# Kernel optimization log

Measured on AMD Instinct MI355X. Metric: run time of the kernel, lower is better.

## Reference

```python
import jax, jax.numpy as jnp
import numpy as np

B, S, IN, H, E, OUT = 64, 2048, 256, 512, 256, 32000


def setup_inputs() -> dict:
    key = jax.random.key(0)
    ks = jax.random.split(key, 20)
    g = lambda k, shp, fan_in: jax.random.normal(k, shp, jnp.float32) / jnp.sqrt(jnp.float32(fan_in))
    return {
        "x": jax.random.normal(ks[0], (B, IN), jnp.float32),
        "hidden": jax.random.normal(ks[1], (B, H), jnp.float32),
        "encoder_outputs": jax.random.normal(ks[2], (B, S, H), jnp.float32),
        # attention params
        "W1_w": g(ks[3], (H, E), H), "W1_b": jnp.zeros((E,), jnp.float32),
        "W2_w": g(ks[4], (H, E), H),
        "v_w": g(ks[5], (E, 1), E),
        # GRU gate params (input to gates is concat(x, context): IN+H)
        "Wxr_w": g(ks[6], (IN + H, H), IN + H), "Wxr_b": jnp.zeros((H,), jnp.float32),
        "Whr_w": g(ks[7], (H, H), H),
        "Wxz_w": g(ks[8], (IN + H, H), IN + H), "Wxz_b": jnp.zeros((H,), jnp.float32),
        "Whz_w": g(ks[9], (H, H), H),
        "Wxh_w": g(ks[10], (IN + H, H), IN + H), "Wxh_b": jnp.zeros((H,), jnp.float32),
        "Whh_w": g(ks[11], (H, H), H),
        # output projection
        "Who_w": g(ks[12], (H, OUT), H), "Who_b": jnp.zeros((OUT,), jnp.float32),
    }


def reference(x, hidden, encoder_outputs,
              W1_w, W1_b, W2_w, v_w,
              Wxr_w, Wxr_b, Whr_w,
              Wxz_w, Wxz_b, Whz_w,
              Wxh_w, Wxh_b, Whh_w,
              Who_w, Who_b):
    # Bahdanau attention
    # energy: [B, S, E]
    energy = jnp.tanh(jnp.einsum("bsh,he->bse", encoder_outputs, W1_w) + W1_b
                      + (hidden @ W2_w)[:, None, :])
    scores = jnp.einsum("bse,eo->bs", energy, v_w)          # [B, S]
    attn_weights = jax.nn.softmax(scores, axis=1)            # [B, S]
    context = jnp.einsum("bs,bsh->bh", attn_weights, encoder_outputs)  # [B, H]

    x_context = jnp.concatenate([x, context], axis=-1)       # [B, IN+H]
    reset_gate = jax.nn.sigmoid(x_context @ Wxr_w + Wxr_b + hidden @ Whr_w)
    update_gate = jax.nn.sigmoid(x_context @ Wxz_w + Wxz_b + hidden @ Whz_w)
    h_tilde = jnp.tanh(x_context @ Wxh_w + Wxh_b + (reset_gate * hidden) @ Whh_w)
    new_hidden = update_gate * hidden + (1.0 - update_gate) * h_tilde
    output = new_hidden @ Who_w + Who_b                      # [B, OUT]
    return (output, new_hidden, attn_weights)
```

## Files before the change

### kernel.cpp

```cpp
#include <hip/hip_runtime.h>

#define BB 64
#define SS 2048
#define INDIM 256
#define HH 512
#define EE 256
#define OUTD 32000

typedef __attribute__((ext_vector_type(8))) short short8;
typedef __attribute__((ext_vector_type(4))) float floatx4;

#define LOG2E 1.4426950408889634f

__device__ __forceinline__ unsigned short f2bf(float f) {
  unsigned u = __float_as_uint(f);
  return (unsigned short)((u + 0x7FFFu + ((u >> 16) & 1u)) >> 16);
}
__device__ __forceinline__ unsigned pk2(float a, float b) {
  return (unsigned)f2bf(a) | ((unsigned)f2bf(b) << 16);
}
__device__ __forceinline__ float bf2f(unsigned short u) {
  return __uint_as_float((unsigned)u << 16);
}
__device__ __forceinline__ float fast_tanh(float x) {
  float e = __builtin_amdgcn_exp2f(x * 2.8853900817779268f);
  return 1.0f - 2.0f * __builtin_amdgcn_rcpf(e + 1.0f);
}
__device__ __forceinline__ float fast_sigmoid(float x) {
  float e = __builtin_amdgcn_exp2f(-x * LOG2E);
  return __builtin_amdgcn_rcpf(1.0f + e);
}

#define WS_W1T   0
#define WS_HBP   262144
#define WS_CTX   393216
#define WS_NHBF  524288
#define WS_Z     589824
#define WS_RH    720896
#define WS_GP    851968
#define WS_NP    3473408
#define WS_CTXP  4784128
#define WS_SUMP  8978432

__global__ void k_prep(const float* __restrict__ W1, unsigned short* __restrict__ W1t) {
  int idx = blockIdx.x * 256 + threadIdx.x;
  int k = idx >> 8, e = idx & 255;
  W1t[e * HH + k] = f2bf(W1[idx]);
}

__global__ __launch_bounds__(256) void k_hb(const float* __restrict__ hidden,
                                            const float* __restrict__ W2,
                                            const float* __restrict__ W1b,
                                            float* __restrict__ hbp) {
  int b0 = blockIdx.x * 4, seg = blockIdx.y, e = threadIdx.x;
  int h0 = seg * 256;
  float a0 = 0, a1 = 0, a2 = 0, a3 = 0;
  if (seg == 0) { a0 = a1 = a2 = a3 = W1b[e]; }
  for (int h = 0; h < 256; ++h) {
    float w = W2[(h0 + h) * EE + e];
    a0 += hidden[(b0 + 0) * HH + h0 + h] * w;
    a1 += hidden[(b0 + 1) * HH + h0 + h] * w;
    a2 += hidden[(b0 + 2) * HH + h0 + h] * w;
    a3 += hidden[(b0 + 3) * HH + h0 + h] * w;
  }
  float* o = hbp + (size_t)seg * BB * EE;
  o[(b0 + 0) * EE + e] = a0; o[(b0 + 1) * EE + e] = a1;
  o[(b0 + 2) * EE + e] = a2; o[(b0 + 3) * EE + e] = a3;
}

#define LDA 520
__global__ __launch_bounds__(256) void k_scores(
    const float* __restrict__ enc, const unsigned short* __restrict__ W1t,
    const float* __restrict__ hbp, const float* __restrict__ vw,
    float* __restrict__ attn, float* __restrict__ ctxp, float* __restrict__ sump) {
  __shared__ unsigned short Afull[64 * LDA];
  __shared__ float hb_s[EE], v_s[EE];
  __shared__ float red[4 * 64];
  __shared__ float wbuf[64];
  __shared__ float redc[4 * 512];

  int tid = threadIdx.x;
  int m0 = blockIdx.x * 64;
  int b = blockIdx.x >> 5;
  int sloc = (blockIdx.x & 31) * 64;
  hb_s[tid] = hbp[b * EE + tid] + hbp[BB * EE + b * EE + tid];
  v_s[tid] = vw[tid];

  int lane = tid & 63, wn = tid >> 6;
  int l15 = lane & 15, quad = lane >> 4;

  int row0 = tid >> 3, kg = tid & 7;
  const float* base0 = enc + (size_t)(m0 + row0) * HH + kg * 4;
  const float* base1 = enc + (size_t)(m0 + 32 + row0) * HH + kg * 4;

  floatx4 acc[4][4];
#pragma unroll
  for (int i = 0; i < 4; ++i)
#pragma unroll
    for (int j = 0; j < 4; ++j) acc[i][j] = (floatx4)0.0f;

  float4 pf0[3], pf1[3];
#pragma unroll
  for (int d = 0; d < 3; ++d) {
    pf0[d] = *(const float4*)(base0 + d * 32);
    pf1[d] = *(const float4*)(base1 + d * 32);
  }

  short8 bcur[4];
#pragma unroll
  for (int j = 0; j < 4; ++j)
    bcur[j] = *(const short8*)(W1t + (wn * 64 + j * 16 + l15) * HH + quad * 8);

#pragma unroll
  for (int kb = 0; kb < 16; ++kb) {
    int slot = kb % 3;
    {
      float4 f = pf0[slot];
      uint2 w; w.x = pk2(f.x, f.y); w.y = pk2(f.z, f.w);
      *(uint2*)(Afull + row0 * LDA + kb * 32 + kg * 4) = w;
      f = pf1[slot];
      uint2 w2; w2.x = pk2(f.x, f.y); w2.y = pk2(f.z, f.w);
      *(uint2*)(Afull + (row0 + 32) * LDA + kb * 32 + kg * 4) = w2;
    }
    if (kb + 3 < 16) {
      pf0[slot] = *(const float4*)(base0 + (kb + 3) * 32);
      pf1[slot] = *(const float4*)(base1 + (kb + 3) * 32);
    }
    short8 bnx[4];
    if (kb + 1 < 16) {
      int kkn = (kb + 1) * 32 + quad * 8;
#pragma unroll
      for (int j = 0; j < 4; ++j)
        bnx[j] = *(const short8*)(W1t + (wn * 64 + j * 16 + l15) * HH + kkn);
    }
    asm volatile("s_waitcnt lgkmcnt(0)" ::: "memory");
    __builtin_amdgcn_s_barrier();
    int kk = kb * 32 + quad * 8;
    short8 a[4];
#pragma unroll
    for (int i = 0; i < 4; ++i)
      a[i] = *(const short8*)(Afull + (i * 16 + l15) * LDA + kk);
#pragma unroll
    for (int j = 0; j < 4; ++j)
#pragma unroll
      for (int i = 0; i < 4; ++i)
        acc[i][j] = __builtin_amdgcn_mfma_f32_16x16x32_bf16(a[i], bcur[j], acc[i][j], 0, 0, 0);
    if (kb + 1 < 16) {
#pragma unroll
      for (int j = 0; j < 4; ++j) bcur[j] = bnx[j];
    }
  }
  __syncthreads();

#pragma unroll
  for (int i = 0; i < 4; ++i)
#pragma unroll
    for (int r = 0; r < 4; ++r) {
      float s = 0.0f;
#pragma unroll
      for (int j = 0; j < 4; ++j) {
        int e = wn * 64 + j * 16 + l15;
        s += fast_tanh(acc[i][j][r] + hb_s[e]) * v_s[e];
      }
#pragma unroll
      for (int off = 1; off < 16; off <<= 1) s += __shfl_xor(s, off, 64);
      if (l15 == 0) red[wn * 64 + i * 16 + quad * 4 + r] = s;
    }
  __syncthreads();
  if (tid < 64) {
    float sc = red[tid] + red[64 + tid] + red[128 + tid] + red[192 + tid];
    float e = __builtin_amdgcn_exp2f(sc * LOG2E);
    wbuf[tid] = e;
    attn[b * SS + sloc + tid] = e;
    float s = e;
#pragma unroll
    for (int off = 1; off < 64; off <<= 1) s += __shfl_xor(s, off, 64);
    if (tid == 0) sump[blockIdx.x] = s;
  }
  __syncthreads();

  float cacc[8];
#pragma unroll
  for (int j = 0; j < 8; ++j) cacc[j] = 0.0f;
#pragma unroll
  for (int rr = 0; rr < 16; ++rr) {
    int r = wn * 16 + rr;
    float w = wbuf[r];
    short8 av = *(const short8*)(Afull + r * LDA + lane * 8);
#pragma unroll
    for (int j = 0; j < 8; ++j) cacc[j] += w * bf2f((unsigned short)av[j]);
  }
#pragma unroll
  for (int j = 0; j < 8; ++j) redc[wn * 512 + lane * 8 + j] = cacc[j];
  __syncthreads();
  float cx0 = redc[tid] + redc[512 + tid] + redc[1024 + tid] + redc[1536 + tid];
  float cx1 = redc[256 + tid] + redc[768 + tid] + redc[1280 + tid] + redc[1792 + tid];
  ctxp[(size_t)blockIdx.x * HH + tid] = cx0;
  ctxp[(size_t)blockIdx.x * HH + 256 + tid] = cx1;
}

__global__ __launch_bounds__(512) void k_norm(float* __restrict__ attn,
                                              const float* __restrict__ ctxp,
                                              const float* __restrict__ sump,
                                              float* __restrict__ ctx) {
  int b = blockIdx.x, tid = threadIdx.x;
  float s = 0.0f;
#pragma unroll
  for (int t = 0; t < 32; ++t) s += sump[b * 32 + t];
  float inv = 1.0f / s;
#pragma unroll
  for (int i = 0; i < 4; ++i) attn[b * SS + tid + i * 512] *= inv;
  float c = 0.0f;
#pragma unroll
  for (int t = 0; t < 32; ++t) c += ctxp[(size_t)(b * 32 + t) * HH + tid];
  ctx[b * HH + tid] = c * inv;
}

__device__ __forceinline__ void part_seg(
    const float* __restrict__ Wx, const float* __restrict__ Wh,
    const float* __restrict__ x, const float* __restrict__ ctx,
    const float* __restrict__ hv, int seg, int b0, int h,
    float* __restrict__ outp) {
  const float* wseg;
  const float* a0; const float* a1; const float* a2; const float* a3;
  int vk0 = seg * 128;
  if (seg < 2) {
    wseg = Wx + (size_t)vk0 * HH;
    a0 = x + (b0 + 0) * INDIM + vk0;       a1 = x + (b0 + 1) * INDIM + vk0;
    a2 = x + (b0 + 2) * INDIM + vk0;       a3 = x + (b0 + 3) * INDIM + vk0;
  } else if (seg < 6) {
    wseg = Wx + (size_t)vk0 * HH;
    int off = vk0 - 256;
    a0 = ctx + (b0 + 0) * HH + off;        a1 = ctx + (b0 + 1) * HH + off;
    a2 = ctx + (b0 + 2) * HH + off;        a3 = ctx + (b0 + 3) * HH + off;
  } else {
    int off = vk0 - 768;
    wseg = Wh + (size_t)off * HH;
    a0 = hv + (b0 + 0) * HH + off;         a1 = hv + (b0 + 1) * HH + off;
    a2 = hv + (b0 + 2) * HH + off;         a3 = hv + (b0 + 3) * HH + off;
  }
  float s0 = 0, s1 = 0, s2 = 0, s3 = 0;
  for (int i = 0; i < 128; ++i) {
    float w = wseg[i * HH + h];
    s0 += a0[i] * w; s1 += a1[i] * w;
    s2 += a2[i] * w; s3 += a3[i] * w;
  }
  outp[(b0 + 0) * HH + h] = s0; outp[(b0 + 1) * HH + h] = s1;
  outp[(b0 + 2) * HH + h] = s2; outp[(b0 + 3) * HH + h] = s3;
}

__global__ __launch_bounds__(512) void k_gpart(
    const float* __restrict__ x, const float* __restrict__ ctx,
    const float* __restrict__ hidden,
    const float* __restrict__ Wxr, const float* __restrict__ Whr,
    const float* __restrict__ Wxz, const float* __restrict__ Whz,
    float* __restrict__ gp) {
  int b0 = blockIdx.x * 4, seg = blockIdx.y, sel = blockIdx.z, h = threadIdx.x;
  const float* Wx = sel ? Wxz : Wxr;
  const float* Wh = sel ? Whz : Whr;
  float* outp = gp + (size_t)(sel * 10 + seg) * BB * HH;
  part_seg(Wx, Wh, x, ctx, hidden, seg, b0, h, outp);
}

__global__ __launch_bounds__(512) void k_gred(
    const float* __restrict__ gp, const float* __restrict__ Wxrb,
    const float* __restrict__ Wxzb, const float* __restrict__ hidden,
    float* __restrict__ z_out, float* __restrict__ rh_out) {
  int b = blockIdx.x, h = threadIdx.x;
  float r = Wxrb[h], z = Wxzb[h];
#pragma unroll
  for (int s = 0; s < 10; ++s) {
    r += gp[((size_t)s * BB + b) * HH + h];
    z += gp[((size_t)(10 + s) * BB + b) * HH + h];
  }
  r = fast_sigmoid(r);
  z_out[b * HH + h] = fast_sigmoid(z);
  rh_out[b * HH + h] = r * hidden[b * HH + h];
}

__global__ __launch_bounds__(512) void k_npart(
    const float* __restrict__ x, const float* __restrict__ ctx,
    const float* __restrict__ rh,
    const float* __restrict__ Wxh, const float* __restrict__ Whh,
    float* __restrict__ np) {
  int b0 = blockIdx.x * 4, seg = blockIdx.y, h = threadIdx.x;
  float* outp = np + (size_t)seg * BB * HH;
  part_seg(Wxh, Whh, x, ctx, rh, seg, b0, h, outp);
}

__global__ __launch_bounds__(512) void k_nred(
    const float* __restrict__ np, const float* __restrict__ Wxhb,
    const float* __restrict__ z, const float* __restrict__ hidden,
    float* __restrict__ nh, unsigned short* __restrict__ nhbf) {
  int b = blockIdx.x, h = threadIdx.x;
  float a = Wxhb[h];
#pragma unroll
  for (int s = 0; s < 10; ++s) a += np[((size_t)s * BB + b) * HH + h];
  float ht = fast_tanh(a);
  float zz = z[b * HH + h];
  float val = zz * hidden[b * HH + h] + (1.0f - zz) * ht;
  nh[b * HH + h] = val;
  nhbf[b * HH + h] = f2bf(val);
}

__global__ __launch_bounds__(256) void k_out2(const unsigned short* __restrict__ nhbf,
                                              const float* __restrict__ Who,
                                              const float* __restrict__ Whob,
                                              float* __restrict__ out) {
  int tid = threadIdx.x;
  int lane = tid & 63, w = tid >> 6;
  int l15 = lane & 15, quad = lane >> 4;
  int n = blockIdx.x * 64 + w * 16 + l15;

  floatx4 acc[4];
#pragma unroll
  for (int i = 0; i < 4; ++i) acc[i] = (floatx4)0.0f;

#pragma unroll
  for (int kc = 0; kc < 16; ++kc) {
    int k0 = kc * 32;
    float bf[8];
    const float* bp = Who + (size_t)(k0 + quad * 8) * OUTD + n;
#pragma unroll
    for (int j = 0; j < 8; ++j) bf[j] = bp[(size_t)j * OUTD];
    union { unsigned u[4]; short8 v; } bu;
#pragma unroll
    for (int j = 0; j < 4; ++j) bu.u[j] = pk2(bf[2 * j], bf[2 * j + 1]);
#pragma unroll
    for (int i = 0; i < 4; ++i) {
      short8 af = *(const short8*)(nhbf + (i * 16 + l15) * HH + k0 + quad * 8);
      acc[i] = __builtin_amdgcn_mfma_f32_16x16x32_bf16(af, bu.v, acc[i], 0, 0, 0);
    }
  }
  float bias = Whob[n];
#pragma unroll
  for (int i = 0; i < 4; ++i)
#pragma unroll
    for (int r = 0; r < 4; ++r) {
      int m = i * 16 + quad * 4 + r;
      out[(size_t)m * OUTD + n] = acc[i][r] + bias;
    }
}

extern "C" void kernel_launch(void* const* d_in, const int* in_sizes, int n_in,
                              void* d_out, int out_size, void* d_ws, size_t ws_size,
                              hipStream_t stream) {
  const float* x    = (const float*)d_in[0];
  const float* hid  = (const float*)d_in[1];
  const float* enc  = (const float*)d_in[2];
  const float* W1w  = (const float*)d_in[3];
  const float* W1b  = (const float*)d_in[4];
  const float* W2w  = (const float*)d_in[5];
  const float* vw   = (const float*)d_in[6];
  const float* Wxr  = (const float*)d_in[7];
  const float* Wxrb = (const float*)d_in[8];
  const float* Whr  = (const float*)d_in[9];
  const float* Wxz  = (const float*)d_in[10];
  const float* Wxzb = (const float*)d_in[11];
  const float* Whz  = (const float*)d_in[12];
  const float* Wxh  = (const float*)d_in[13];
  const float* Wxhb = (const float*)d_in[14];
  const float* Whh  = (const float*)d_in[15];
  const float* Who  = (const float*)d_in[16];
  const float* Whob = (const float*)d_in[17];

  float* out  = (float*)d_out;
  float* nh   = out + (size_t)BB * OUTD;
  float* attn = nh + (size_t)BB * HH;

  char* ws = (char*)d_ws;
  unsigned short* W1t  = (unsigned short*)(ws + WS_W1T);
  float* hbp  = (float*)(ws + WS_HBP);
  float* ctx  = (float*)(ws + WS_CTX);
  unsigned short* nhbf = (unsigned short*)(ws + WS_NHBF);
  float* zg   = (float*)(ws + WS_Z);
  float* rh   = (float*)(ws + WS_RH);
  float* gp   = (float*)(ws + WS_GP);
  float* np   = (float*)(ws + WS_NP);
  float* ctxp = (float*)(ws + WS_CTXP);
  float* sump = (float*)(ws + WS_SUMP);

  k_prep<<<512, 256, 0, stream>>>(W1w, W1t);
  k_hb<<<dim3(16, 2), 256, 0, stream>>>(hid, W2w, W1b, hbp);
  k_scores<<<(BB * SS) / 64, 256, 0, stream>>>(enc, W1t, hbp, vw, attn, ctxp, sump);
  k_norm<<<BB, 512, 0, stream>>>(attn, ctxp, sump, ctx);
  k_gpart<<<dim3(16, 10, 2), 512, 0, stream>>>(x, ctx, hid, Wxr, Whr, Wxz, Whz, gp);
  k_gred<<<BB, 512, 0, stream>>>(gp, Wxrb, Wxzb, hid, zg, rh);
  k_npart<<<dim3(16, 10), 512, 0, stream>>>(x, ctx, rh, Wxh, Whh, np);
  k_nred<<<BB, 512, 0, stream>>>(np, Wxhb, zg, hid, nh, nhbf);
  k_out2<<<500, 256, 0, stream>>>(nhbf, Who, Whob, out);
}
```

Before: 527.6 us.

## Halve k_scores tile to 32 rows and write per-wave context partials

Cuts the k_scores row tile from 64 to 32 rows, doubling the grid and shrinking shared memory and accumulator registers so more blocks fit per CU (launch bounds 256,4). The prefetch depth over the encoder tile grows to 6 float4s per thread. The cross-wave context reduction through shared memory is removed: each wave writes its own partial context vector to global memory, so k_norm now sums 256 partials per batch instead of 32. This adds workspace traffic, roughly 32 MB of ctx partials written and then re-read, and more W1t B-operand reloads per row in exchange for better occupancy and latency hiding.

Result: slower. 608.9 us (+15.4%).

```diff
diff --git a/kernel.cpp b/kernel.cpp
--- a/kernel.cpp
+++ b/kernel.cpp
@@ -40,7 +40,7 @@
 #define WS_GP    851968
 #define WS_NP    3473408
 #define WS_CTXP  4784128
-#define WS_SUMP  8978432
+#define WS_SUMP  38338560
 
 __global__ void k_prep(const float* __restrict__ W1, unsigned short* __restrict__ W1t) {
   int idx = blockIdx.x * 256 + threadIdx.x;
@@ -69,20 +69,19 @@
 }
 
 #define LDA 520
-__global__ __launch_bounds__(256) void k_scores(
+__global__ __launch_bounds__(256, 4) void k_scores(
     const float* __restrict__ enc, const unsigned short* __restrict__ W1t,
     const float* __restrict__ hbp, const float* __restrict__ vw,
     float* __restrict__ attn, float* __restrict__ ctxp, float* __restrict__ sump) {
-  __shared__ unsigned short Afull[64 * LDA];
+  __shared__ unsigned short Afull[32 * LDA];
   __shared__ float hb_s[EE], v_s[EE];
-  __shared__ float red[4 * 64];
-  __shared__ float wbuf[64];
-  __shared__ float redc[4 * 512];
+  __shared__ float red[4 * 32];
+  __shared__ float wbuf[32];
 
   int tid = threadIdx.x;
-  int m0 = blockIdx.x * 64;
-  int b = blockIdx.x >> 5;
-  int sloc = (blockIdx.x & 31) * 64;
+  int m0 = blockIdx.x * 32;
+  int b = blockIdx.x >> 6;
+  int sloc = (blockIdx.x & 63) * 32;
   hb_s[tid] = hbp[b * EE + tid] + hbp[BB * EE + b * EE + tid];
   v_s[tid] = vw[tid];
 
@@ -91,20 +90,16 @@
 
   int row0 = tid >> 3, kg = tid & 7;
   const float* base0 = enc + (size_t)(m0 + row0) * HH + kg * 4;
-  const float* base1 = enc + (size_t)(m0 + 32 + row0) * HH + kg * 4;
-
-  floatx4 acc[4][4];
-#pragma unroll
-  for (int i = 0; i < 4; ++i)
+
+  floatx4 acc[2][4];
+#pragma unroll
+  for (int i = 0; i < 2; ++i)
 #pragma unroll
     for (int j = 0; j < 4; ++j) acc[i][j] = (floatx4)0.0f;
 
-  float4 pf0[3], pf1[3];
-#pragma unroll
-  for (int d = 0; d < 3; ++d) {
-    pf0[d] = *(const float4*)(base0 + d * 32);
-    pf1[d] = *(const float4*)(base1 + d * 32);
-  }
+  float4 pf[6];
+#pragma unroll
+  for (int d = 0; d < 6; ++d) pf[d] = *(const float4*)(base0 + d * 32);
 
   short8 bcur[4];
 #pragma unroll
@@ -113,19 +108,13 @@
 
 #pragma unroll
   for (int kb = 0; kb < 16; ++kb) {
-    int slot = kb % 3;
+    int slot = kb % 6;
     {
-      float4 f = pf0[slot];
+      float4 f = pf[slot];
       uint2 w; w.x = pk2(f.x, f.y); w.y = pk2(f.z, f.w);
       *(uint2*)(Afull + row0 * LDA + kb * 32 + kg * 4) = w;
-      f = pf1[slot];
-      uint2 w2; w2.x = pk2(f.x, f.y); w2.y = pk2(f.z, f.w);
-      *(uint2*)(Afull + (row0 + 32) * LDA + kb * 32 + kg * 4) = w2;
-    }
-    if (kb + 3 < 16) {
-      pf0[slot] = *(const float4*)(base0 + (kb + 3) * 32);
-      pf1[slot] = *(const float4*)(base1 + (kb + 3) * 32);
-    }
+    }
+    if (kb + 6 < 16) pf[slot] = *(const float4*)(base0 + (kb + 6) * 32);
     short8 bnx[4];
     if (kb + 1 < 16) {
       int kkn = (kb + 1) * 32 + quad * 8;
@@ -136,15 +125,13 @@
     asm volatile("s_waitcnt lgkmcnt(0)" ::: "memory");
     __builtin_amdgcn_s_barrier();
     int kk = kb * 32 + quad * 8;
-    short8 a[4];
-#pragma unroll
-    for (int i = 0; i < 4; ++i)
-      a[i] = *(const short8*)(Afull + (i * 16 + l15) * LDA + kk);
-#pragma unroll
-    for (int j = 0; j < 4; ++j)
-#pragma unroll
-      for (int i = 0; i < 4; ++i)
-        acc[i][j] = __builtin_amdgcn_mfma_f32_16x16x32_bf16(a[i], bcur[j], acc[i][j], 0, 0, 0);
+    short8 a0v = *(const short8*)(Afull + l15 * LDA + kk);
+    short8 a1v = *(const short8*)(Afull + (16 + l15) * LDA + kk);
+#pragma unroll
+    for (int j = 0; j < 4; ++j) {
+      acc[0][j] = __builtin_amdgcn_mfma_f32_16x16x32_bf16(a0v, bcur[j], acc[0][j], 0, 0, 0);
+      acc[1][j] = __builtin_amdgcn_mfma_f32_16x16x32_bf16(a1v, bcur[j], acc[1][j], 0, 0, 0);
+    }
     if (kb + 1 < 16) {
 #pragma unroll
       for (int j = 0; j < 4; ++j) bcur[j] = bnx[j];
@@ -153,7 +140,7 @@
   __syncthreads();
 
 #pragma unroll
-  for (int i = 0; i < 4; ++i)
+  for (int i = 0; i < 2; ++i)
 #pragma unroll
     for (int r = 0; r < 4; ++r) {
       float s = 0.0f;
@@ -164,17 +151,17 @@
       }
 #pragma unroll
       for (int off = 1; off < 16; off <<= 1) s += __shfl_xor(s, off, 64);
-      if (l15 == 0) red[wn * 64 + i * 16 + quad * 4 + r] = s;
+      if (l15 == 0) red[wn * 32 + i * 16 + quad * 4 + r] = s;
     }
   __syncthreads();
-  if (tid < 64) {
-    float sc = red[tid] + red[64 + tid] + red[128 + tid] + red[192 + tid];
+  if (tid < 32) {
+    float sc = red[tid] + red[32 + tid] + red[64 + tid] + red[96 + tid];
     float e = __builtin_amdgcn_exp2f(sc * LOG2E);
     wbuf[tid] = e;
     attn[b * SS + sloc + tid] = e;
     float s = e;
 #pragma unroll
-    for (int off = 1; off < 64; off <<= 1) s += __shfl_xor(s, off, 64);
+    for (int off = 1; off < 32; off <<= 1) s += __shfl_xor(s, off, 64);
     if (tid == 0) sump[blockIdx.x] = s;
   }
   __syncthreads();
@@ -183,20 +170,19 @@
 #pragma unroll
   for (int j = 0; j < 8; ++j) cacc[j] = 0.0f;
 #pragma unroll
-  for (int rr = 0; rr < 16; ++rr) {
-    int r = wn * 16 + rr;
+  for (int rr = 0; rr < 8; ++rr) {
+    int r = wn * 8 + rr;
     float w = wbuf[r];
     short8 av = *(const short8*)(Afull + r * LDA + lane * 8);
 #pragma unroll
     for (int j = 0; j < 8; ++j) cacc[j] += w * bf2f((unsigned short)av[j]);
   }
-#pragma unroll
-  for (int j = 0; j < 8; ++j) redc[wn * 512 + lane * 8 + j] = cacc[j];
-  __syncthreads();
-  float cx0 = redc[tid] + redc[512 + tid] + redc[1024 + tid] + redc[1536 + tid];
-  float cx1 = redc[256 + tid] + redc[768 + tid] + redc[1280 + tid] + redc[1792 + tid];
-  ctxp[(size_t)blockIdx.x * HH + tid] = cx0;
-  ctxp[(size_t)blockIdx.x * HH + 256 + tid] = cx1;
+  float4 c0, c1;
+  c0.x = cacc[0]; c0.y = cacc[1]; c0.z = cacc[2]; c0.w = cacc[3];
+  c1.x = cacc[4]; c1.y = cacc[5]; c1.z = cacc[6]; c1.w = cacc[7];
+  float* cp = ctxp + ((size_t)blockIdx.x * 4 + wn) * HH + lane * 8;
+  *(float4*)cp = c0;
+  *(float4*)(cp + 4) = c1;
 }
 
 __global__ __launch_bounds__(512) void k_norm(float* __restrict__ attn,
@@ -206,13 +192,13 @@
   int b = blockIdx.x, tid = threadIdx.x;
   float s = 0.0f;
 #pragma unroll
-  for (int t = 0; t < 32; ++t) s += sump[b * 32 + t];
+  for (int t = 0; t < 64; ++t) s += sump[b * 64 + t];
   float inv = 1.0f / s;
 #pragma unroll
   for (int i = 0; i < 4; ++i) attn[b * SS + tid + i * 512] *= inv;
   float c = 0.0f;
-#pragma unroll
-  for (int t = 0; t < 32; ++t) c += ctxp[(size_t)(b * 32 + t) * HH + tid];
+#pragma unroll 8
+  for (int t = 0; t < 256; ++t) c += ctxp[(size_t)(b * 256 + t) * HH + tid];
   ctx[b * HH + tid] = c * inv;
 }
 
@@ -382,7 +368,7 @@
 
   k_prep<<<512, 256, 0, stream>>>(W1w, W1t);
   k_hb<<<dim3(16, 2), 256, 0, stream>>>(hid, W2w, W1b, hbp);
-  k_scores<<<(BB * SS) / 64, 256, 0, stream>>>(enc, W1t, hbp, vw, attn, ctxp, sump);
+  k_scores<<<(BB * SS) / 32, 256, 0, stream>>>(enc, W1t, hbp, vw, attn, ctxp, sump);
   k_norm<<<BB, 512, 0, stream>>>(attn, ctxp, sump, ctx);
   k_gpart<<<dim3(16, 10, 2), 512, 0, stream>>>(x, ctx, hid, Wxr, Whr, Wxz, Whz, gp);
   k_gred<<<BB, 512, 0, stream>>>(gp, Wxrb, Wxzb, hid, zg, rh);
```
